# Kernel tuning notes

Measured on AMD Instinct MI355X. Metric: run time of the kernel, lower is better.

## Reference

```python
import jax, jax.numpy as jnp
import numpy as np

B, N, K_H, K_EC = 32, 2048, 50, 5  # graphs, nodes/graph, homophily-knn k, edgeconv k


def _leaky(v):
    return jnp.where(v >= 0, v, 0.01 * v)


def _pairwise_sq(xg):
    # xg: [B,N,F] -> squared euclidean distances [B,N,N]
    s = jnp.sum(xg * xg, axis=-1)
    return s[:, :, None] + s[:, None, :] - 2.0 * jnp.einsum('bnf,bmf->bnm', xg, xg)


def _gather(xg, idx):
    # xg [B,N,F], idx [B,N,k] -> [B,N,k,F]
    return jax.vmap(lambda xs, ix: xs[ix])(xg, idx)


def _edge_conv(xg, w1, b1, w2, b2):
    # DynamicEdgeConv: knn (self included, as PyG knn), msg = nn([x_i, x_j - x_i]), aggr='add'
    d = _pairwise_sq(xg)
    _, idx = jax.lax.top_k(-d, K_EC)          # [B,N,k]
    xj = _gather(xg, idx)                      # [B,N,k,F]
    xi = jnp.broadcast_to(xg[:, :, None, :], xj.shape)
    m = jnp.concatenate([xi, xj - xi], axis=-1)
    h = _leaky(m @ w1 + b1)
    h = _leaky(h @ w2 + b2)
    return h.sum(axis=2)                       # add aggregation -> [B,N,out]


def _homophily(y, idx):
    # y [B,N], idx [B,N,k]: fraction of edges whose endpoints have equal value, per graph
    yj = jax.vmap(lambda ys, ix: ys[ix])(y, idx)
    same = (yj == y[:, :, None]).astype(jnp.float32)
    return same.mean(axis=(1, 2))              # [B]


def reference(x, pos, batch, c1w1, c1b1, c1w2, c1b2, c2w1, c2b1, c2w2, c2b2,
              l1w1, l1b1, l1w2, l1b2, mw1, mb1, mw2, mb2):
    xx = jnp.concatenate([x, pos], axis=1).reshape(B, N, 4)
    # homophily kNN graph (k=50, self-loops excluded as in knn_graph)
    d = _pairwise_sq(xx) + jnp.eye(N, dtype=xx.dtype) * 1e9
    _, hidx = jax.lax.top_k(-d, K_H)
    h = [_homophily(xx[..., c], hidx) for c in range(4)]  # hx,hy,hz,hq each [B]
    x1 = _edge_conv(xx, c1w1, c1b1, c1w2, c1b2)   # [B,N,64]
    x2 = _edge_conv(x1, c2w1, c2b1, c2w2, c2b2)   # shared conv2 weights
    x3 = _edge_conv(x2, c2w1, c2b1, c2w2, c2b2)
    feat = jnp.concatenate([xx, x1, x2, x3], axis=-1)  # [B,N,196]
    o = _leaky(feat @ l1w1 + l1b1) @ l1w2 + l1b2       # lin1 -> [B,N,256]
    o = o.mean(axis=1)                                  # global_mean_pool -> [B,256]
    o = jnp.concatenate([o] + [hh[:, None] for hh in h], axis=1)  # [B,260]
    o = _leaky(o)
    o = _leaky(o @ mw1 + mb1)
    return o @ mw2 + mb2                                # [B,cla]


def setup_inputs() -> dict:
    key = jax.random.key(0)
    ks = jax.random.split(key, 20)

    def lin(k, fin, fout):
        kw, kb = jax.random.split(k)
        s = 1.0 / np.sqrt(fin)
        return (jax.random.uniform(kw, (fin, fout), jnp.float32, -s, s),
                jax.random.uniform(kb, (fout,), jnp.float32, -s, s))

    x = jax.random.normal(ks[0], (B * N, 1), jnp.float32)
    pos = jax.random.normal(ks[1], (B * N, 3), jnp.float32)
    batch = jnp.repeat(jnp.arange(B, dtype=jnp.int64), N)
    c1w1, c1b1 = lin(ks[2], 8, 64)
    c1w2, c1b2 = lin(ks[3], 64, 64)
    c2w1, c2b1 = lin(ks[4], 128, 128)
    c2w2, c2b2 = lin(ks[5], 128, 64)
    l1w1, l1b1 = lin(ks[6], 196, 512)
    l1w2, l1b2 = lin(ks[7], 512, 256)
    mw1, mb1 = lin(ks[8], 260, 256)
    mw2, mb2 = lin(ks[9], 256, 3)
    return dict(x=x, pos=pos, batch=batch,
                c1w1=c1w1, c1b1=c1b1, c1w2=c1w2, c1b2=c1b2,
                c2w1=c2w1, c2b1=c2b1, c2w2=c2w2, c2b2=c2b2,
                l1w1=l1w1, l1b1=l1b1, l1w2=l1w2, l1b2=l1b2,
                mw1=mw1, mb1=mb1, mw2=mw2, mb2=mb2)
```

## Files before the change

### kernel.cpp

```cpp
#include <hip/hip_runtime.h>

static constexpr int B = 32, N = 2048, BN = B * N;

#define DEV static __device__ __forceinline__

typedef _Float16 half_t;
typedef __attribute__((ext_vector_type(8))) _Float16 half8;
typedef __attribute__((ext_vector_type(4))) float f32x4;
typedef unsigned long long u64;

DEV float lk(float v) { return v >= 0.f ? v : 0.01f * v; }
DEV bool lexlt(float d1, int j1, float d2, int j2) {
    return d1 < d2 || (d1 == d2 && j1 < j2);
}

DEV unsigned int mono(float f) {
    unsigned int b = __float_as_uint(f);
    return b ^ ((unsigned int)((int)b >> 31) | 0x80000000u);
}
DEV float unmono(unsigned int v) {
    unsigned int b = (v & 0x80000000u) ? (v & 0x7fffffffu) : ~v;
    return __uint_as_float(b);
}
DEV u64 pk(float d, int j) {
    return ((u64)mono(d) << 32) | (unsigned int)j;
}
static constexpr u64 KINIT = 0xFF800000ull << 32 | 0x7fffffffull;

DEV int mbcnt64(unsigned long long m) {
    return __builtin_amdgcn_mbcnt_hi((unsigned)(m >> 32),
                                     __builtin_amdgcn_mbcnt_lo((unsigned)m, 0));
}
DEV float dist4s(float4 a, float sa, float4 b, float sb) {
    float dt = fmaf(a.x, b.x, fmaf(a.y, b.y, fmaf(a.z, b.z, a.w * b.w)));
    return (sa + sb) - 2.f * dt;
}

__global__ __launch_bounds__(256) void k_build_xx(const float* __restrict__ x,
                                                  const float* __restrict__ pos,
                                                  float* __restrict__ xx,
                                                  float* __restrict__ sq) {
    int i = blockIdx.x * 256 + threadIdx.x;
    if (i < BN) {
        float4 v;
        v.x = x[i];
        v.y = pos[3 * i + 0];
        v.z = pos[3 * i + 1];
        v.w = pos[3 * i + 2];
        ((float4*)xx)[i] = v;
        sq[i] = fmaf(v.x, v.x, fmaf(v.y, v.y, fmaf(v.z, v.z, v.w * v.w)));
    }
}

__global__ __launch_bounds__(256, 8) void k_knn4(const float* __restrict__ xx,
                                                 const float* __restrict__ sq,
                                                 int* __restrict__ c1idx,
                                                 unsigned int* __restrict__ hpart) {
    int gw = (blockIdx.x * 256 + threadIdx.x) >> 6;
    int lane = threadIdx.x & 63;
    int g = gw >> 11, i = gw & 2047;
    int lane_self = i & 63, t_self = i >> 6;
    const float4* base = ((const float4*)xx) + g * N;
    const float* sqb = sq + g * N;
    float4 xi = base[i];
    float si = sqb[i];

    unsigned int u[32];
    unsigned int L[6];
    unsigned int eqany = 0;
#pragma unroll
    for (int s = 0; s < 6; s++) L[s] = 0xFFFFFFFFu;
#pragma unroll 4
    for (int t = 0; t < 32; t++) {
        float4 xj = base[lane + 64 * t];
        float sj = sqb[lane + 64 * t];
        unsigned int nv = mono(dist4s(xi, si, xj, sj));
        u[t] = nv;
        bool eq = (xj.x == xi.x) | (xj.y == xi.y) | (xj.z == xi.z) | (xj.w == xi.w);
        bool notself = (lane + 64 * t) != i;
        eqany |= (eq && notself) ? (1u << t) : 0u;
#pragma unroll
        for (int s = 0; s < 6; s++) {
            unsigned int lo_ = min(L[s], nv);
            nv = max(L[s], nv);
            L[s] = lo_;
        }
    }
    unsigned int uself = 0x80000000u;
    bool haveEq = (__ballot(eqany != 0) != 0ULL);

    unsigned int lo = L[0], hi = L[0];
#pragma unroll
    for (int o = 1; o < 64; o <<= 1) {
        lo = min(lo, (unsigned int)__shfl_xor((int)lo, o));
        hi = max(hi, (unsigned int)__shfl_xor((int)hi, o));
    }
    unsigned int cp = lo ^ hi;
    int msb = cp ? (31 - __builtin_clz(cp)) : -1;
    unsigned int prefix = (msb >= 0) ? (hi & ~((2u << msb) - 1u)) : lo;

    unsigned int vA = prefix, vB = prefix;
    if (haveEq) {
#pragma unroll 1
        for (int bit = msb; bit >= 0; --bit) {
            unsigned int cA = vA | (1u << bit);
            unsigned int cB = vB | (1u << bit);
            int cntA = 0, cntB = 0;
#pragma unroll
            for (int s = 0; s < 6; s++) cntA += (int)__popcll(__ballot(L[s] < cA));
#pragma unroll
            for (int s = 0; s < 5; s++) cntB += (int)__popcll(__ballot(L[s] < cB));
            cntA -= (uself < cA) ? 1 : 0;
            if (cntA < 50) vA = cA;
            if (cntB < 5) vB = cB;
        }
        if (__ballot(L[5] < vA) != 0ULL) {
            vA = prefix;
#pragma unroll 1
            for (int bit = msb; bit >= 0; --bit) {
                unsigned int c = vA | (1u << bit);
                int cnt = 0;
#pragma unroll
                for (int t = 0; t < 32; t++) cnt += (int)__popcll(__ballot(u[t] < c));
                cnt -= (uself < c) ? 1 : 0;
                if (cnt < 50) vA = c;
            }
        }
    } else {
#pragma unroll 1
        for (int bit = msb; bit >= 0; --bit) {
            unsigned int cB = vB | (1u << bit);
            int cntB = 0;
#pragma unroll
            for (int s = 0; s < 5; s++) cntB += (int)__popcll(__ballot(L[s] < cB));
            if (cntB < 5) vB = cB;
        }
    }

    unsigned int rawB = 0, eqBm = 0;
#pragma unroll
    for (int t = 0; t < 32; t++) {
        rawB |= (u[t] < vB ? 1u : 0u) << t;
        eqBm |= (u[t] == vB ? 1u : 0u) << t;
    }
    unsigned int packB = (unsigned)__popc(rawB) | ((unsigned)__popc(eqBm) << 16);

    if (haveEq) {
        unsigned int rawA = 0, eqAm = 0;
#pragma unroll
        for (int t = 0; t < 32; t++) {
            rawA |= (u[t] < vA ? 1u : 0u) << t;
            eqAm |= (u[t] == vA ? 1u : 0u) << t;
        }
        unsigned int packA = (unsigned)__popc(rawA) | ((unsigned)__popc(eqAm) << 16);
#pragma unroll
        for (int o = 1; o < 64; o <<= 1) packA += __shfl_xor(packA, o);
        int cltA = (int)(packA & 0xffffu) - ((uself < vA) ? 1 : 0);
        int ceqA = (int)(packA >> 16) - ((uself == vA) ? 1 : 0);

        int neededA = 50 - cltA;
        bool allEqA = (ceqA == neededA);
        unsigned int selAm = rawA, eqAs = eqAm;
        if (lane == lane_self) {
            selAm &= ~(1u << t_self);
            eqAs &= ~(1u << t_self);
        }
        unsigned int hm = allEqA ? (selAm | eqAs) : selAm;
        int c0 = 0, c1 = 0, c2 = 0, c3 = 0;
        unsigned int mm = hm;
        while (mm) {
            int t = __ffs(mm) - 1;
            mm &= mm - 1;
            float4 xj = base[lane + 64 * t];
            c0 += (xj.x == xi.x) ? 1 : 0;
            c1 += (xj.y == xi.y) ? 1 : 0;
            c2 += (xj.z == xi.z) ? 1 : 0;
            c3 += (xj.w == xi.w) ? 1 : 0;
        }
        if (!allEqA) {
            unsigned int em = eqAs;
            for (int r = 0; r < neededA; r++) {
                int mt = __ffs(em) - 1;
                int mj = (mt >= 0) ? (lane + 64 * mt) : 0x7fffffff;
                int bm = mj;
#pragma unroll
                for (int o = 1; o < 64; o <<= 1) bm = min(bm, __shfl_xor(bm, o));
                if (mj == bm && mt >= 0) {
                    em &= ~(1u << mt);
                    float4 xj = base[lane + 64 * mt];
                    c0 += (xj.x == xi.x) ? 1 : 0;
                    c1 += (xj.y == xi.y) ? 1 : 0;
                    c2 += (xj.z == xi.z) ? 1 : 0;
                    c3 += (xj.w == xi.w) ? 1 : 0;
                }
            }
        }
        unsigned int pc = (unsigned)c0 | ((unsigned)c1 << 8) | ((unsigned)c2 << 16) | ((unsigned)c3 << 24);
#pragma unroll
        for (int o = 1; o < 64; o <<= 1) pc += __shfl_xor(pc, o);
        if (lane == 0) hpart[gw] = pc;
    } else {
        if (lane == 0) hpart[gw] = 0u;
    }

#pragma unroll
    for (int o = 1; o < 64; o <<= 1) packB += __shfl_xor(packB, o);
    int cltB = (int)(packB & 0xffffu);
    int ceqB = (int)(packB >> 16);
    int neededB = 5 - cltB;
    bool allEqB = (ceqB == neededB);
    unsigned int selBm = allEqB ? (rawB | eqBm) : rawB;
    int base_slot = 0;
#pragma unroll 4
    for (int t = 0; t < 32; t++) {
        bool take = (selBm >> t) & 1;
        unsigned long long m = __ballot(take);
        if (take) c1idx[gw * 5 + base_slot + mbcnt64(m)] = lane + 64 * t;
        base_slot += (int)__popcll(m);
    }
    if (!allEqB) {
        unsigned int em = eqBm;
        for (int r = 0; r < neededB; r++) {
            int mt = __ffs(em) - 1;
            int mj = (mt >= 0) ? (lane + 64 * mt) : 0x7fffffff;
            int bm = mj;
#pragma unroll
            for (int o = 1; o < 64; o <<= 1) bm = min(bm, __shfl_xor(bm, o));
            if (mj == bm && mt >= 0) {
                em &= ~(1u << mt);
                c1idx[gw * 5 + base_slot + r] = bm;
            }
        }
    }
}

__global__ __launch_bounds__(256) void k_split(const float* __restrict__ X,
                                               half_t* __restrict__ Xh,
                                               half_t* __restrict__ Xl,
                                               float* __restrict__ s) {
    int row = (blockIdx.x * 256 + threadIdx.x) >> 6;
    int lane = threadIdx.x & 63;
    float x = X[(size_t)row * 64 + lane];
    half_t h = (half_t)x;
    half_t l = (half_t)(x - (float)h);
    Xh[(size_t)row * 64 + lane] = h;
    Xl[(size_t)row * 64 + lane] = l;
    float ss = x * x;
#pragma unroll
    for (int o = 1; o < 64; o <<= 1) ss += __shfl_xor(ss, o);
    if (lane == 0) s[row] = ss;
}

template <int F, int C>
__global__ __launch_bounds__(256, 4) void k_pq(const float* __restrict__ X,
                                               const float* __restrict__ w1,
                                               const float* __restrict__ b1,
                                               float* __restrict__ p,
                                               float* __restrict__ q) {
    constexpr int FS = F + 4;
    __shared__ __align__(16) float Xs[64 * FS];
    __shared__ __align__(16) float Ws[64 * FS];
    int nbase = blockIdx.x * 64;
    int cchunk = blockIdx.y;
    int tx = threadIdx.x & 15, ty = threadIdx.x >> 4;
    for (int idx = threadIdx.x; idx < 64 * (F / 4); idx += 256) {
        int r = idx / (F / 4), fq = idx % (F / 4);
        float4 v = ((const float4*)(X + (size_t)(nbase + r) * F))[fq];
        *(float4*)&Xs[r * FS + fq * 4] = v;
    }
    for (int idx = threadIdx.x; idx < 64 * F; idx += 256) {
        int f = idx >> 6, cl = idx & 63;
        int ccg = cchunk * 64 + cl;
        float v;
        if (ccg < C) v = w1[f * C + ccg] - w1[(F + f) * C + ccg];
        else         v = w1[(F + f) * C + (ccg - C)];
        Ws[cl * FS + f] = v;
    }
    __syncthreads();
    float acc[4][4];
#pragma unroll
    for (int a = 0; a < 4; a++)
#pragma unroll
        for (int b = 0; b < 4; b++) acc[a][b] = 0.f;
#pragma unroll 2
    for (int fs = 0; fs < F / 4; fs++) {
        float4 xv[4], wv[4];
#pragma unroll
        for (int a = 0; a < 4; a++) xv[a] = *(const float4*)&Xs[(ty + 16 * a) * FS + fs * 4];
#pragma unroll
        for (int b = 0; b < 4; b++) wv[b] = *(const float4*)&Ws[(tx + 16 * b) * FS + fs * 4];
#pragma unroll
        for (int a = 0; a < 4; a++)
#pragma unroll
            for (int b = 0; b < 4; b++) {
                acc[a][b] = fmaf(xv[a].x, wv[b].x, acc[a][b]);
                acc[a][b] = fmaf(xv[a].y, wv[b].y, acc[a][b]);
                acc[a][b] = fmaf(xv[a].z, wv[b].z, acc[a][b]);
                acc[a][b] = fmaf(xv[a].w, wv[b].w, acc[a][b]);
            }
    }
#pragma unroll
    for (int a = 0; a < 4; a++) {
        int n = nbase + ty + 16 * a;
#pragma unroll
        for (int b = 0; b < 4; b++) {
            int ccg = cchunk * 64 + tx + 16 * b;
            if (ccg < C) p[(size_t)n * C + ccg] = acc[a][b] + b1[ccg];
            else         q[(size_t)n * C + (ccg - C)] = acc[a][b];
        }
    }
}

template <int C1>
__global__ __launch_bounds__(256, 4) void k_edge(const float* __restrict__ p,
                                                 const float* __restrict__ q,
                                                 const int* __restrict__ cidx,
                                                 const float* __restrict__ w2,
                                                 const float* __restrict__ b2,
                                                 float* __restrict__ Xout) {
    __shared__ __align__(16) float h1[80 * 68];
    __shared__ __align__(16) float w2T[64 * 68];
    int nb = blockIdx.x * 16;
    int gb = (nb >> 11) << 11;
    int tx = threadIdx.x & 15, ty = threadIdx.x >> 4;
    float acc[5][4];
#pragma unroll
    for (int m = 0; m < 5; m++)
#pragma unroll
        for (int n = 0; n < 4; n++) acc[m][n] = 0.f;
#pragma unroll 1
    for (int half = 0; half < C1 / 64; half++) {
        __syncthreads();
        for (int idx = threadIdx.x; idx < 64 * 64; idx += 256) {
            int l = idx >> 6, c = idx & 63;
            w2T[c * 68 + l] = w2[(half * 64 + l) * 64 + c];
        }
        for (int idx = threadIdx.x; idx < 80 * 16; idx += 256) {
            int e = idx >> 4, fq = idx & 15;
            int node = nb + e / 5, kk = e - 5 * (e / 5);
            int j = cidx[node * 5 + kk];
            float4 pv = ((const float4*)(p + (size_t)node * C1 + half * 64))[fq];
            float4 qv = ((const float4*)(q + (size_t)(gb + j) * C1 + half * 64))[fq];
            float4 hv;
            hv.x = lk(pv.x + qv.x); hv.y = lk(pv.y + qv.y);
            hv.z = lk(pv.z + qv.z); hv.w = lk(pv.w + qv.w);
            *(float4*)&h1[e * 68 + fq * 4] = hv;
        }
        __syncthreads();
#pragma unroll 1
        for (int ls = 0; ls < 16; ls++) {
            float4 hv[5], wf[4];
#pragma unroll
            for (int m = 0; m < 5; m++) hv[m] = *(const float4*)&h1[(ty + 16 * m) * 68 + ls * 4];
#pragma unroll
            for (int n = 0; n < 4; n++) wf[n] = *(const float4*)&w2T[(tx + 16 * n) * 68 + ls * 4];
#pragma unroll
            for (int m = 0; m < 5; m++)
#pragma unroll
                for (int n = 0; n < 4; n++) {
                    acc[m][n] = fmaf(hv[m].x, wf[n].x, acc[m][n]);
                    acc[m][n] = fmaf(hv[m].y, wf[n].y, acc[m][n]);
                    acc[m][n] = fmaf(hv[m].z, wf[n].z, acc[m][n]);
                    acc[m][n] = fmaf(hv[m].w, wf[n].w, acc[m][n]);
                }
        }
    }
    float b2r[4];
#pragma unroll
    for (int n = 0; n < 4; n++) b2r[n] = b2[tx + 16 * n];
    __syncthreads();
    float* h2 = h1;
#pragma unroll
    for (int m = 0; m < 5; m++)
#pragma unroll
        for (int n = 0; n < 4; n++)
            h2[(ty + 16 * m) * 68 + (tx + 16 * n)] = lk(acc[m][n] + b2r[n]);
    __syncthreads();
#pragma unroll
    for (int rr = 0; rr < 4; rr++) {
        int idx = threadIdx.x + 256 * rr;
        int node = idx >> 6, c = idx & 63;
        float sum = 0.f;
#pragma unroll
        for (int kk = 0; kk < 5; kk++) sum += h2[(node * 5 + kk) * 68 + c];
        Xout[(size_t)(nb + node) * 64 + c] = sum;
    }
}

__global__ __launch_bounds__(256) void k_knn64(const half_t* __restrict__ Xh,
                                               const half_t* __restrict__ Xl,
                                               const float* __restrict__ s,
                                               float2* __restrict__ cand) {
    __shared__ __align__(16) char smem[20480];
    int g = blockIdx.x, it = blockIdx.y, bz = blockIdx.z;
    int gbase = g * 2048, ibase = it * 64;
    int lane = threadIdx.x & 63, wave = threadIdx.x >> 6;
    int m = lane & 15, quad = lane >> 4;

    const half_t* ahp = Xh + (size_t)(gbase + ibase + wave * 16 + m) * 64 + quad * 8;
    const half_t* alp = Xl + (size_t)(gbase + ibase + wave * 16 + m) * 64 + quad * 8;
    half8 Ah0 = *(const half8*)(ahp);
    half8 Ah1 = *(const half8*)(ahp + 32);
    half8 Al0 = *(const half8*)(alp);
    half8 Al1 = *(const half8*)(alp + 32);
    float si_r[4];
#pragma unroll
    for (int reg = 0; reg < 4; reg++)
        si_r[reg] = s[gbase + ibase + wave * 16 + quad * 4 + reg];

    u64 K[4][5];
    float thv[4];
#pragma unroll
    for (int a = 0; a < 4; a++) {
        thv[a] = __builtin_inff();
#pragma unroll
        for (int ss = 0; ss < 5; ss++) K[a][ss] = KINIT;
    }

    int jt0 = bz * 8;
    half8 Pbh0[2], Pbh1[2], Pbl0[2], Pbl1[2];
    float Psj[2];
    {
        int jrow = gbase + jt0 * 64 + m;
        const half_t* bhp = Xh + (size_t)jrow * 64 + quad * 8;
        const half_t* blp = Xl + (size_t)jrow * 64 + quad * 8;
        Pbh0[0] = *(const half8*)(bhp);
        Pbh1[0] = *(const half8*)(bhp + 32);
        Pbl0[0] = *(const half8*)(blp);
        Pbl1[0] = *(const half8*)(blp + 32);
        Psj[0] = s[jrow];
    }

#pragma unroll 1
    for (int jtl = 0; jtl < 8; jtl++) {
        int jt = jt0 + jtl;
#pragma unroll
        for (int reg = 0; reg < 4; reg++) {
            float th = unmono((unsigned int)(K[reg][4] >> 32));
            th = fminf(th, __shfl_xor(th, 1));
            th = fminf(th, __shfl_xor(th, 2));
            th = fminf(th, __shfl_xor(th, 4));
            th = fminf(th, __shfl_xor(th, 8));
            thv[reg] = th;
        }
#pragma unroll
        for (int sub = 0; sub < 4; sub++) {
            int cur = sub & 1, nxt = cur ^ 1;
            if (sub < 3 || jtl < 7) {
                int njt = (sub < 3) ? jt : (jt + 1);
                int nsub = (sub < 3) ? (sub + 1) : 0;
                int jrow = gbase + njt * 64 + nsub * 16 + m;
                const half_t* bhp = Xh + (size_t)jrow * 64 + quad * 8;
                const half_t* blp = Xl + (size_t)jrow * 64 + quad * 8;
                Pbh0[nxt] = *(const half8*)(bhp);
                Pbh1[nxt] = *(const half8*)(bhp + 32);
                Pbl0[nxt] = *(const half8*)(blp);
                Pbl1[nxt] = *(const half8*)(blp + 32);
                Psj[nxt] = s[jrow];
            }
            f32x4 ahh = {0.f, 0.f, 0.f, 0.f};
            f32x4 ahl = {0.f, 0.f, 0.f, 0.f};
            f32x4 alh = {0.f, 0.f, 0.f, 0.f};
            f32x4 all = {0.f, 0.f, 0.f, 0.f};
            ahh = __builtin_amdgcn_mfma_f32_16x16x32_f16(Ah0, Pbh0[cur], ahh, 0, 0, 0);
            ahl = __builtin_amdgcn_mfma_f32_16x16x32_f16(Ah0, Pbl0[cur], ahl, 0, 0, 0);
            alh = __builtin_amdgcn_mfma_f32_16x16x32_f16(Al0, Pbh0[cur], alh, 0, 0, 0);
            all = __builtin_amdgcn_mfma_f32_16x16x32_f16(Al0, Pbl0[cur], all, 0, 0, 0);
            ahh = __builtin_amdgcn_mfma_f32_16x16x32_f16(Ah1, Pbh1[cur], ahh, 0, 0, 0);
            ahl = __builtin_amdgcn_mfma_f32_16x16x32_f16(Ah1, Pbl1[cur], ahl, 0, 0, 0);
            alh = __builtin_amdgcn_mfma_f32_16x16x32_f16(Al1, Pbh1[cur], alh, 0, 0, 0);
            all = __builtin_amdgcn_mfma_f32_16x16x32_f16(Al1, Pbl1[cur], all, 0, 0, 0);
            float sjv = Psj[cur];
            int jv = jt * 64 + sub * 16 + m;
#pragma unroll
            for (int reg = 0; reg < 4; reg++) {
                float dot = ((all[reg] + alh[reg]) + ahl[reg]) + ahh[reg];
                float dv = (si_r[reg] + sjv) - 2.f * dot;
                if (__any(dv <= thv[reg])) {
                    if (dv <= thv[reg]) {
                        u64 nk = pk(dv, jv);
                        if (nk < K[reg][4]) {
                            K[reg][4] = nk;
#pragma unroll
                            for (int ss = 4; ss >= 1; ss--)
                                if (K[reg][ss] < K[reg][ss - 1]) {
                                    u64 t = K[reg][ss]; K[reg][ss] = K[reg][ss - 1]; K[reg][ss - 1] = t;
                                }
                        }
                    }
                }
            }
        }
    }

#pragma unroll
    for (int reg = 0; reg < 4; reg++) {
        u64 pv[5];
#pragma unroll
        for (int ss = 0; ss < 5; ss++) pv[ss] = __shfl_xor(K[reg][ss], 1);
        if ((lane & 1) == 0) {
#pragma unroll
            for (int c = 0; c < 5; c++) {
                if (pv[c] < K[reg][4]) {
                    K[reg][4] = pv[c];
#pragma unroll
                    for (int ss = 4; ss >= 1; ss--)
                        if (K[reg][ss] < K[reg][ss - 1]) {
                            u64 t = K[reg][ss]; K[reg][ss] = K[reg][ss - 1]; K[reg][ss - 1] = t;
                        }
                }
            }
        }
    }

    u64* candk = (u64*)smem;
    int rowbase = wave * 16 + quad * 4;
    if ((lane & 1) == 0) {
#pragma unroll
        for (int reg = 0; reg < 4; reg++)
#pragma unroll
            for (int ss = 0; ss < 5; ss++)
                candk[(rowbase + reg) * 40 + (m >> 1) * 5 + ss] = K[reg][ss];
    }
    __syncthreads();
    if (threadIdx.x < 64) {
        int row = threadIdx.x;
        u64 fk[5];
#pragma unroll
        for (int ss = 0; ss < 5; ss++) fk[ss] = KINIT;
#pragma unroll 1
        for (int c = 0; c < 40; c++) {
            u64 k = candk[row * 40 + c];
            if (k < fk[4]) {
                fk[4] = k;
#pragma unroll
                for (int ss = 4; ss >= 1; ss--)
                    if (fk[ss] < fk[ss - 1]) {
                        u64 t = fk[ss]; fk[ss] = fk[ss - 1]; fk[ss - 1] = t;
                    }
            }
        }
#pragma unroll
        for (int ss = 0; ss < 5; ss++) {
            float2 e;
            e.x = unmono((unsigned int)(fk[ss] >> 32));
            e.y = __int_as_float((int)(unsigned int)(fk[ss] & 0xffffffffu));
            cand[((size_t)(gbase + ibase + row) * 4 + bz) * 5 + ss] = e;
        }
    }
}

__global__ __launch_bounds__(256) void k_knn_merge(const float2* __restrict__ cand,
                                                   int* __restrict__ cidx) {
    int row = blockIdx.x * 256 + threadIdx.x;
    if (row >= BN) return;
    float fv[5];
    int fj[5];
#pragma unroll
    for (int ss = 0; ss < 5; ss++) { fv[ss] = __builtin_inff(); fj[ss] = 0x7fffffff; }
#pragma unroll
    for (int c = 0; c < 20; c++) {
        float2 e = cand[(size_t)row * 20 + c];
        float dv = e.x;
        int jv = __float_as_int(e.y);
        if (lexlt(dv, jv, fv[4], fj[4])) {
            fv[4] = dv; fj[4] = jv;
#pragma unroll
            for (int ss = 4; ss >= 1; ss--)
                if (lexlt(fv[ss], fj[ss], fv[ss - 1], fj[ss - 1])) {
                    float tv = fv[ss]; fv[ss] = fv[ss - 1]; fv[ss - 1] = tv;
                    int tj = fj[ss]; fj[ss] = fj[ss - 1]; fj[ss - 1] = tj;
                }
        }
    }
#pragma unroll
    for (int ss = 0; ss < 5; ss++) cidx[(size_t)row * 5 + ss] = fj[ss];
}

__global__ __launch_bounds__(256, 3) void k_lin1(const float* __restrict__ xx,
                                                 const float* __restrict__ x1,
                                                 const float* __restrict__ x2,
                                                 const float* __restrict__ x3,
                                                 const float* __restrict__ w1,
                                                 const float* __restrict__ b1,
                                                 float* __restrict__ Hpart) {
    __shared__ __align__(16) float ft[64 * 100];
    __shared__ __align__(16) float wT[64 * 100];
    int cch = blockIdx.x, g = blockIdx.y, z = blockIdx.z;
    int gbase = g * 2048;
    int tx = threadIdx.x & 15, ty = threadIdx.x >> 4;
    float accp[4][4][4];
#pragma unroll
    for (int nt = 0; nt < 4; nt++)
#pragma unroll
        for (int rm = 0; rm < 4; rm++)
#pragma unroll
            for (int ca = 0; ca < 4; ca++) accp[nt][rm][ca] = 0.f;
#pragma unroll 1
    for (int half = 0; half < 2; half++) {
        int FH = half ? 96 : 100;
        __syncthreads();
        for (int idx = threadIdx.x; idx < 64 * 100; idx += 256) {
            int f = idx >> 6, cl = idx & 63;
            if (f < FH) wT[cl * 100 + f] = w1[(half * 100 + f) * 512 + cch * 64 + cl];
        }
        int NF4 = half ? 24 : 25;
#pragma unroll 1
        for (int nt = 0; nt < 4; nt++) {
            int n0 = (z * 4 + nt) * 64;
            __syncthreads();
            for (int idx = threadIdx.x; idx < 64 * NF4; idx += 256) {
                int r = idx / NF4, fq = idx - r * NF4;
                int node = gbase + n0 + r;
                float4 v;
                if (half == 0) {
                    if (fq == 0)      v = ((const float4*)(xx + (size_t)node * 4))[0];
                    else if (fq < 17) v = ((const float4*)(x1 + (size_t)node * 64))[fq - 1];
                    else              v = ((const float4*)(x2 + (size_t)node * 64))[fq - 17];
                } else {
                    if (fq < 8)       v = ((const float4*)(x2 + (size_t)node * 64))[fq + 8];
                    else              v = ((const float4*)(x3 + (size_t)node * 64))[fq - 8];
                }
                *(float4*)&ft[r * 100 + fq * 4] = v;
            }
            __syncthreads();
            int FSN = NF4;
#pragma unroll 2
            for (int fs = 0; fs < FSN; fs++) {
                float4 fv[4], wv[4];
#pragma unroll
                for (int rm = 0; rm < 4; rm++) fv[rm] = *(const float4*)&ft[(ty + 16 * rm) * 100 + fs * 4];
#pragma unroll
                for (int ca = 0; ca < 4; ca++) wv[ca] = *(const float4*)&wT[(tx + 16 * ca) * 100 + fs * 4];
#pragma unroll
                for (int rm = 0; rm < 4; rm++)
#pragma unroll
                    for (int ca = 0; ca < 4; ca++) {
                        accp[nt][rm][ca] = fmaf(fv[rm].x, wv[ca].x, accp[nt][rm][ca]);
                        accp[nt][rm][ca] = fmaf(fv[rm].y, wv[ca].y, accp[nt][rm][ca]);
                        accp[nt][rm][ca] = fmaf(fv[rm].z, wv[ca].z, accp[nt][rm][ca]);
                        accp[nt][rm][ca] = fmaf(fv[rm].w, wv[ca].w, accp[nt][rm][ca]);
                    }
            }
        }
    }
    float b1r[4];
#pragma unroll
    for (int ca = 0; ca < 4; ca++) b1r[ca] = b1[cch * 64 + tx + 16 * ca];
    float psum[4] = {0.f, 0.f, 0.f, 0.f};
#pragma unroll
    for (int nt = 0; nt < 4; nt++)
#pragma unroll
        for (int rm = 0; rm < 4; rm++)
#pragma unroll
            for (int ca = 0; ca < 4; ca++) psum[ca] += lk(accp[nt][rm][ca] + b1r[ca]);
    __syncthreads();
    float* red = ft;
#pragma unroll
    for (int ca = 0; ca < 4; ca++) red[ty * 64 + tx + 16 * ca] = psum[ca];
    __syncthreads();
    if (threadIdx.x < 64) {
        float tot = 0.f;
#pragma unroll
        for (int t = 0; t < 16; t++) tot += red[t * 64 + threadIdx.x];
        Hpart[((size_t)z * 32 + g) * 512 + cch * 64 + threadIdx.x] = tot;
    }
}

__global__ __launch_bounds__(256) void k_final(const float* __restrict__ Hpart,
                                               const unsigned int* __restrict__ hpart,
                                               const float* __restrict__ l1w2,
                                               const float* __restrict__ l1b2,
                                               const float* __restrict__ mw1,
                                               const float* __restrict__ mb1,
                                               const float* __restrict__ mw2,
                                               const float* __restrict__ mb2,
                                               float* __restrict__ out) {
    __shared__ float Hb[512];
    __shared__ float z[260];
    __shared__ float y[256];
    __shared__ unsigned int hsum[4];
    int g = blockIdx.x, t = threadIdx.x;
    if (t < 4) hsum[t] = 0;
    __syncthreads();
    unsigned int s0 = 0, s1 = 0, s2 = 0, s3 = 0;
#pragma unroll
    for (int r = 0; r < 8; r++) {
        unsigned int v = hpart[g * 2048 + t + 256 * r];
        s0 += v & 0xffu; s1 += (v >> 8) & 0xffu;
        s2 += (v >> 16) & 0xffu; s3 += (v >> 24) & 0xffu;
    }
    atomicAdd(&hsum[0], s0); atomicAdd(&hsum[1], s1);
    atomicAdd(&hsum[2], s2); atomicAdd(&hsum[3], s3);
#pragma unroll
    for (int half = 0; half < 2; half++) {
        int c = t + 256 * half;
        float v = 0.f;
#pragma unroll
        for (int zz = 0; zz < 8; zz++) v += Hpart[((size_t)zz * 32 + g) * 512 + c];
        Hb[c] = v * (1.f / 2048.f);
    }
    __syncthreads();
    float acc = l1b2[t];
    for (int f = 0; f < 512; f++) acc = fmaf(Hb[f], l1w2[f * 256 + t], acc);
    z[t] = lk(acc);
    if (t < 4) z[256 + t] = lk((float)hsum[t] * (1.f / (2048.f * 50.f)));
    __syncthreads();
    float acc2 = mb1[t];
    for (int f = 0; f < 260; f++) acc2 = fmaf(z[f], mw1[f * 256 + t], acc2);
    y[t] = lk(acc2);
    __syncthreads();
    if (t < 3) {
        float a = mb2[t];
        for (int c = 0; c < 256; c++) a = fmaf(y[c], mw2[c * 3 + t], a);
        out[g * 3 + t] = a;
    }
}

extern "C" void kernel_launch(void* const* d_in, const int* in_sizes, int n_in,
                              void* d_out, int out_size, void* d_ws, size_t ws_size,
                              hipStream_t stream) {
    (void)in_sizes; (void)n_in; (void)out_size; (void)ws_size;
    const float* x    = (const float*)d_in[0];
    const float* pos  = (const float*)d_in[1];
    const float* c1w1 = (const float*)d_in[3];
    const float* c1b1 = (const float*)d_in[4];
    const float* c1w2 = (const float*)d_in[5];
    const float* c1b2 = (const float*)d_in[6];
    const float* c2w1 = (const float*)d_in[7];
    const float* c2b1 = (const float*)d_in[8];
    const float* c2w2 = (const float*)d_in[9];
    const float* c2b2 = (const float*)d_in[10];
    const float* l1w1 = (const float*)d_in[11];
    const float* l1b1 = (const float*)d_in[12];
    const float* l1w2 = (const float*)d_in[13];
    const float* l1b2 = (const float*)d_in[14];
    const float* mw1  = (const float*)d_in[15];
    const float* mb1  = (const float*)d_in[16];
    const float* mw2  = (const float*)d_in[17];
    const float* mb2  = (const float*)d_in[18];
    float* out = (float*)d_out;

    char* w = (char*)d_ws;
    auto alloc = [&](size_t bytes) -> void* {
        void* r = (void*)w;
        w += (bytes + 255) & ~(size_t)255;
        return r;
    };
    float* xx   = (float*)alloc((size_t)BN * 4 * 4);
    float* pbuf = (float*)alloc((size_t)BN * 128 * 4);
    float* qbuf = (float*)alloc((size_t)BN * 128 * 4);
    float* x1   = (float*)alloc((size_t)BN * 64 * 4);
    float* x2   = (float*)alloc((size_t)BN * 64 * 4);
    float* x3   = (float*)alloc((size_t)BN * 64 * 4);
    float* sbuf = (float*)alloc((size_t)BN * 4);
    float* sq4  = (float*)alloc((size_t)BN * 4);
    half_t* xh  = (half_t*)alloc((size_t)BN * 64 * 2);
    half_t* xl  = (half_t*)alloc((size_t)BN * 64 * 2);
    int* c1i    = (int*)alloc((size_t)BN * 5 * 4);
    int* c2i    = (int*)alloc((size_t)BN * 5 * 4);
    int* c3i    = (int*)alloc((size_t)BN * 5 * 4);
    unsigned int* hpart = (unsigned int*)alloc((size_t)BN * 4);
    float* Hpart = (float*)alloc((size_t)8 * 32 * 512 * 4);
    float2* cand = (float2*)alloc((size_t)BN * 20 * 8);

    k_build_xx<<<BN / 256, 256, 0, stream>>>(x, pos, xx, sq4);
    k_knn4<<<BN / 4, 256, 0, stream>>>(xx, sq4, c1i, hpart);
    k_pq<4, 64><<<dim3(BN / 64, 2), 256, 0, stream>>>(xx, c1w1, c1b1, pbuf, qbuf);
    k_edge<64><<<BN / 16, 256, 0, stream>>>(pbuf, qbuf, c1i, c1w2, c1b2, x1);
    k_split<<<BN / 4, 256, 0, stream>>>(x1, xh, xl, sbuf);
    k_knn64<<<dim3(32, 32, 4), 256, 0, stream>>>(xh, xl, sbuf, cand);
    k_knn_merge<<<BN / 256, 256, 0, stream>>>(cand, c2i);
    k_pq<64, 128><<<dim3(BN / 64, 4), 256, 0, stream>>>(x1, c2w1, c2b1, pbuf, qbuf);
    k_edge<128><<<BN / 16, 256, 0, stream>>>(pbuf, qbuf, c2i, c2w2, c2b2, x2);
    k_split<<<BN / 4, 256, 0, stream>>>(x2, xh, xl, sbuf);
    k_knn64<<<dim3(32, 32, 4), 256, 0, stream>>>(xh, xl, sbuf, cand);
    k_knn_merge<<<BN / 256, 256, 0, stream>>>(cand, c3i);
    k_pq<64, 128><<<dim3(BN / 64, 4), 256, 0, stream>>>(x2, c2w1, c2b1, pbuf, qbuf);
    k_edge<128><<<BN / 16, 256, 0, stream>>>(pbuf, qbuf, c3i, c2w2, c2b2, x3);
    k_lin1<<<dim3(8, 32, 8), 256, 0, stream>>>(xx, x1, x2, x3, l1w1, l1b1, Hpart);
    k_final<<<32, 256, 0, stream>>>(Hpart, hpart, l1w2, l1b2, mw1, mb1, mw2, mb2, out);
}
```

Measured before the change: 1.540 ms.

## Move lin1 GEMM to MFMA using split-fp16 hi/lo operands

Replaces the fp32 FMA lin1 kernel with an MFMA 16x16x32 f16 kernel. Features and weights are first split into high and low fp16 halves and padded to K=224, and three MFMAs per step (hi*hi, hi*lo, lo*hi) approximate fp32 precision. The bias, leaky ReLU and mean-pool partial sums are fused into the epilogue, with 32 partial slices per graph. The aim is to cut the FP32 ALU cost of the 65536x196x512 GEMM, at the price of two extra conversion kernels, extra memory traffic for the split buffers, and a small loss of precision.

```diff
diff --git a/kernel.cpp b/kernel.cpp
--- a/kernel.cpp
+++ b/kernel.cpp
@@ -6,6 +6,7 @@
 
 typedef _Float16 half_t;
 typedef __attribute__((ext_vector_type(8))) _Float16 half8;
+typedef __attribute__((ext_vector_type(4))) _Float16 half4;
 typedef __attribute__((ext_vector_type(4))) float f32x4;
 typedef unsigned long long u64;
 
@@ -577,93 +578,97 @@
     for (int ss = 0; ss < 5; ss++) cidx[(size_t)row * 5 + ss] = fj[ss];
 }
 
-__global__ __launch_bounds__(256, 3) void k_lin1(const float* __restrict__ xx,
-                                                 const float* __restrict__ x1,
-                                                 const float* __restrict__ x2,
-                                                 const float* __restrict__ x3,
-                                                 const float* __restrict__ w1,
-                                                 const float* __restrict__ b1,
-                                                 float* __restrict__ Hpart) {
-    __shared__ __align__(16) float ft[64 * 100];
-    __shared__ __align__(16) float wT[64 * 100];
-    int cch = blockIdx.x, g = blockIdx.y, z = blockIdx.z;
-    int gbase = g * 2048;
-    int tx = threadIdx.x & 15, ty = threadIdx.x >> 4;
-    float accp[4][4][4];
-#pragma unroll
-    for (int nt = 0; nt < 4; nt++)
-#pragma unroll
-        for (int rm = 0; rm < 4; rm++)
-#pragma unroll
-            for (int ca = 0; ca < 4; ca++) accp[nt][rm][ca] = 0.f;
+__global__ __launch_bounds__(256) void k_wsplit(const float* __restrict__ w1,
+                                                half_t* __restrict__ WhT,
+                                                half_t* __restrict__ WlT) {
+    int idx = blockIdx.x * 256 + threadIdx.x;
+    if (idx >= 512 * 224) return;
+    int c = idx / 224, f = idx - c * 224;
+    float v = (f < 196) ? w1[(size_t)f * 512 + c] : 0.f;
+    half_t h = (half_t)v;
+    WhT[(size_t)c * 224 + f] = h;
+    WlT[(size_t)c * 224 + f] = (half_t)(v - (float)h);
+}
+
+__global__ __launch_bounds__(256) void k_fsplit(const float* __restrict__ xx,
+                                                const float* __restrict__ x1,
+                                                const float* __restrict__ x2,
+                                                const float* __restrict__ x3,
+                                                half_t* __restrict__ Fh,
+                                                half_t* __restrict__ Fl) {
+    int nb = blockIdx.x * 64;
+    for (int idx = threadIdx.x; idx < 64 * 56; idx += 256) {
+        int r = idx / 56, sg = idx - r * 56;
+        int node = nb + r;
+        float4 v;
+        if (sg == 0)       v = ((const float4*)xx)[node];
+        else if (sg < 17)  v = ((const float4*)(x1 + (size_t)node * 64))[sg - 1];
+        else if (sg < 33)  v = ((const float4*)(x2 + (size_t)node * 64))[sg - 17];
+        else if (sg < 49)  v = ((const float4*)(x3 + (size_t)node * 64))[sg - 33];
+        else { v.x = 0.f; v.y = 0.f; v.z = 0.f; v.w = 0.f; }
+        float f0 = v.x, f1 = v.y, f2 = v.z, f3 = v.w;
+        half_t h0 = (half_t)f0, h1 = (half_t)f1, h2 = (half_t)f2, h3 = (half_t)f3;
+        half4 hv = {h0, h1, h2, h3};
+        half4 lv = {(half_t)(f0 - (float)h0), (half_t)(f1 - (float)h1),
+                    (half_t)(f2 - (float)h2), (half_t)(f3 - (float)h3)};
+        *(half4*)(Fh + (size_t)node * 224 + sg * 4) = hv;
+        *(half4*)(Fl + (size_t)node * 224 + sg * 4) = lv;
+    }
+}
+
+__global__ __launch_bounds__(256) void k_lin1m(const half_t* __restrict__ Fh,
+                                               const half_t* __restrict__ Fl,
+                                               const half_t* __restrict__ WhT,
+                                               const half_t* __restrict__ WlT,
+                                               const float* __restrict__ b1,
+                                               float* __restrict__ Hpart) {
+    __shared__ __align__(16) half_t Bh[16 * 232];
+    __shared__ __align__(16) half_t Bl[16 * 232];
+    __shared__ float pool[4][512];
+    int zb = blockIdx.x, g = blockIdx.y;
+    int lane = threadIdx.x & 63, wave = threadIdx.x >> 6;
+    int m = lane & 15, quad = lane >> 4;
+    for (int i = threadIdx.x; i < 4 * 512; i += 256) ((float*)pool)[i] = 0.f;
+    int node = g * 2048 + zb * 64 + wave * 16 + m;
+    const half_t* fh = Fh + (size_t)node * 224 + quad * 8;
+    const half_t* fl = Fl + (size_t)node * 224 + quad * 8;
+    half8 Ah[7], Al[7];
+#pragma unroll
+    for (int ks = 0; ks < 7; ks++) {
+        Ah[ks] = *(const half8*)(fh + ks * 32);
+        Al[ks] = *(const half8*)(fl + ks * 32);
+    }
+    __syncthreads();
 #pragma unroll 1
-    for (int half = 0; half < 2; half++) {
-        int FH = half ? 96 : 100;
+    for (int ct = 0; ct < 32; ct++) {
+        for (int idx = threadIdx.x; idx < 448; idx += 256) {
+            int r = idx / 28, cc = idx - r * 28;
+            *(half8*)&Bh[r * 232 + cc * 8] = *(const half8*)(WhT + (size_t)(ct * 16 + r) * 224 + cc * 8);
+            *(half8*)&Bl[r * 232 + cc * 8] = *(const half8*)(WlT + (size_t)(ct * 16 + r) * 224 + cc * 8);
+        }
         __syncthreads();
-        for (int idx = threadIdx.x; idx < 64 * 100; idx += 256) {
-            int f = idx >> 6, cl = idx & 63;
-            if (f < FH) wT[cl * 100 + f] = w1[(half * 100 + f) * 512 + cch * 64 + cl];
-        }
-        int NF4 = half ? 24 : 25;
-#pragma unroll 1
-        for (int nt = 0; nt < 4; nt++) {
-            int n0 = (z * 4 + nt) * 64;
-            __syncthreads();
-            for (int idx = threadIdx.x; idx < 64 * NF4; idx += 256) {
-                int r = idx / NF4, fq = idx - r * NF4;
-                int node = gbase + n0 + r;
-                float4 v;
-                if (half == 0) {
-                    if (fq == 0)      v = ((const float4*)(xx + (size_t)node * 4))[0];
-                    else if (fq < 17) v = ((const float4*)(x1 + (size_t)node * 64))[fq - 1];
-                    else              v = ((const float4*)(x2 + (size_t)node * 64))[fq - 17];
-                } else {
-                    if (fq < 8)       v = ((const float4*)(x2 + (size_t)node * 64))[fq + 8];
-                    else              v = ((const float4*)(x3 + (size_t)node * 64))[fq - 8];
-                }
-                *(float4*)&ft[r * 100 + fq * 4] = v;
-            }
-            __syncthreads();
-            int FSN = NF4;
-#pragma unroll 2
-            for (int fs = 0; fs < FSN; fs++) {
-                float4 fv[4], wv[4];
-#pragma unroll
-                for (int rm = 0; rm < 4; rm++) fv[rm] = *(const float4*)&ft[(ty + 16 * rm) * 100 + fs * 4];
-#pragma unroll
-                for (int ca = 0; ca < 4; ca++) wv[ca] = *(const float4*)&wT[(tx + 16 * ca) * 100 + fs * 4];
-#pragma unroll
-                for (int rm = 0; rm < 4; rm++)
-#pragma unroll
-                    for (int ca = 0; ca < 4; ca++) {
-                        accp[nt][rm][ca] = fmaf(fv[rm].x, wv[ca].x, accp[nt][rm][ca]);
-                        accp[nt][rm][ca] = fmaf(fv[rm].y, wv[ca].y, accp[nt][rm][ca]);
-                        accp[nt][rm][ca] = fmaf(fv[rm].z, wv[ca].z, accp[nt][rm][ca]);
-                        accp[nt][rm][ca] = fmaf(fv[rm].w, wv[ca].w, accp[nt][rm][ca]);
-                    }
-            }
-        }
-    }
-    float b1r[4];
-#pragma unroll
-    for (int ca = 0; ca < 4; ca++) b1r[ca] = b1[cch * 64 + tx + 16 * ca];
-    float psum[4] = {0.f, 0.f, 0.f, 0.f};
-#pragma unroll
-    for (int nt = 0; nt < 4; nt++)
-#pragma unroll
-        for (int rm = 0; rm < 4; rm++)
-#pragma unroll
-            for (int ca = 0; ca < 4; ca++) psum[ca] += lk(accp[nt][rm][ca] + b1r[ca]);
-    __syncthreads();
-    float* red = ft;
-#pragma unroll
-    for (int ca = 0; ca < 4; ca++) red[ty * 64 + tx + 16 * ca] = psum[ca];
-    __syncthreads();
-    if (threadIdx.x < 64) {
-        float tot = 0.f;
-#pragma unroll
-        for (int t = 0; t < 16; t++) tot += red[t * 64 + threadIdx.x];
-        Hpart[((size_t)z * 32 + g) * 512 + cch * 64 + threadIdx.x] = tot;
+        f32x4 a1 = {0.f, 0.f, 0.f, 0.f};
+        f32x4 a2 = {0.f, 0.f, 0.f, 0.f};
+#pragma unroll
+        for (int ks = 0; ks < 7; ks++) {
+            half8 bh = *(const half8*)&Bh[m * 232 + ks * 32 + quad * 8];
+            half8 bl = *(const half8*)&Bl[m * 232 + ks * 32 + quad * 8];
+            a1 = __builtin_amdgcn_mfma_f32_16x16x32_f16(Ah[ks], bh, a1, 0, 0, 0);
+            a2 = __builtin_amdgcn_mfma_f32_16x16x32_f16(Ah[ks], bl, a2, 0, 0, 0);
+            a2 = __builtin_amdgcn_mfma_f32_16x16x32_f16(Al[ks], bh, a2, 0, 0, 0);
+        }
+        float bb = b1[ct * 16 + m];
+        float sacc = 0.f;
+#pragma unroll
+        for (int reg = 0; reg < 4; reg++) sacc += lk((a1[reg] + a2[reg]) + bb);
+        sacc += __shfl_xor(sacc, 16);
+        sacc += __shfl_xor(sacc, 32);
+        if (quad == 0) pool[wave][ct * 16 + m] += sacc;
+        __syncthreads();
+    }
+    for (int c = threadIdx.x; c < 512; c += 256) {
+        float v = pool[0][c] + pool[1][c] + pool[2][c] + pool[3][c];
+        Hpart[((size_t)zb * 32 + g) * 512 + c] = v;
     }
 }
 
@@ -697,7 +702,7 @@
         int c = t + 256 * half;
         float v = 0.f;
 #pragma unroll
-        for (int zz = 0; zz < 8; zz++) v += Hpart[((size_t)zz * 32 + g) * 512 + c];
+        for (int zz = 0; zz < 32; zz++) v += Hpart[((size_t)zz * 32 + g) * 512 + c];
         Hb[c] = v * (1.f / 2048.f);
     }
     __syncthreads();
@@ -761,10 +766,15 @@
     int* c2i    = (int*)alloc((size_t)BN * 5 * 4);
     int* c3i    = (int*)alloc((size_t)BN * 5 * 4);
     unsigned int* hpart = (unsigned int*)alloc((size_t)BN * 4);
-    float* Hpart = (float*)alloc((size_t)8 * 32 * 512 * 4);
+    float* Hpart = (float*)alloc((size_t)32 * 32 * 512 * 4);
     float2* cand = (float2*)alloc((size_t)BN * 20 * 8);
+    half_t* Fh  = (half_t*)alloc((size_t)BN * 224 * 2);
+    half_t* Fl  = (half_t*)alloc((size_t)BN * 224 * 2);
+    half_t* WhT = (half_t*)alloc((size_t)512 * 224 * 2);
+    half_t* WlT = (half_t*)alloc((size_t)512 * 224 * 2);
 
     k_build_xx<<<BN / 256, 256, 0, stream>>>(x, pos, xx, sq4);
+    k_wsplit<<<(512 * 224 + 255) / 256, 256, 0, stream>>>(l1w1, WhT, WlT);
     k_knn4<<<BN / 4, 256, 0, stream>>>(xx, sq4, c1i, hpart);
     k_pq<4, 64><<<dim3(BN / 64, 2), 256, 0, stream>>>(xx, c1w1, c1b1, pbuf, qbuf);
     k_edge<64><<<BN / 16, 256, 0, stream>>>(pbuf, qbuf, c1i, c1w2, c1b2, x1);
@@ -778,6 +788,7 @@
     k_knn_merge<<<BN / 256, 256, 0, stream>>>(cand, c3i);
     k_pq<64, 128><<<dim3(BN / 64, 4), 256, 0, stream>>>(x2, c2w1, c2b1, pbuf, qbuf);
     k_edge<128><<<BN / 16, 256, 0, stream>>>(pbuf, qbuf, c3i, c2w2, c2b2, x3);
-    k_lin1<<<dim3(8, 32, 8), 256, 0, stream>>>(xx, x1, x2, x3, l1w1, l1b1, Hpart);
+    k_fsplit<<<BN / 64, 256, 0, stream>>>(xx, x1, x2, x3, Fh, Fl);
+    k_lin1m<<<dim3(32, 32), 256, 0, stream>>>(Fh, Fl, WhT, WlT, l1b1, Hpart);
     k_final<<<32, 256, 0, stream>>>(Hpart, hpart, l1w2, l1b2, mw1, mb1, mw2, mb2, out);
 }
```

Measured after the change: 1.370 ms. 11.0% less time.
